# Kernel optimization log

Measured on AMD Instinct MI355X. Metric: run time of the kernel, lower is better.

The kernel has to match this reference:

```python
import jax, jax.numpy as jnp
import numpy as np

POOL = 7
IMG_DIM = 1024.0
NUM_CLASSES = 81
EPS = 1e-3


def crop_and_resize(fmap, boxes, P):
    """TF-style crop_and_resize with extrapolation_value=0.
    fmap: [C,H,W] (all box_indices are 0 in the original), boxes: [R,4] normalized (y1,x1,y2,x2).
    Returns [R,C,P,P]."""
    C, H, W = fmap.shape
    y1, x1, y2, x2 = boxes[:, 0], boxes[:, 1], boxes[:, 2], boxes[:, 3]
    g = jnp.arange(P, dtype=fmap.dtype) / (P - 1)  # [P]
    ys = y1[:, None] * (H - 1) + g[None, :] * ((y2 - y1) * (H - 1))[:, None]  # [R,P]
    xs = x1[:, None] * (W - 1) + g[None, :] * ((x2 - x1) * (W - 1))[:, None]  # [R,P]

    def axis(coords, size):
        valid = (coords >= 0) & (coords <= size - 1)
        c = jnp.clip(coords, 0, size - 1)
        lo = jnp.floor(c)
        hi = jnp.minimum(lo + 1, size - 1)
        return lo.astype(jnp.int32), hi.astype(jnp.int32), c - lo, valid

    y_lo, y_hi, wy, vy = axis(ys, H)
    x_lo, x_hi, wx, vx = axis(xs, W)

    def gather(yi, xi):  # -> [C,R,P,P]
        return fmap[:, yi[:, :, None], xi[:, None, :]]

    wxe = wx[None, :, None, :]
    top = gather(y_lo, x_lo) * (1 - wxe) + gather(y_lo, x_hi) * wxe
    bot = gather(y_hi, x_lo) * (1 - wxe) + gather(y_hi, x_hi) * wxe
    wye = wy[None, :, :, None]
    out = top * (1 - wye) + bot * wye
    mask = (vy[:, :, None] & vx[:, None, :])[None]  # [1,R,P,P]
    out = jnp.where(mask, out, jnp.zeros((), fmap.dtype))
    return jnp.transpose(out, (1, 0, 2, 3))  # [R,C,P,P]


def roi_align(fmaps, rois_flat):
    """rois_flat: [R,4] pixel coords (x1,y1,x2,y2). fmaps: list of 4 [C,H,W] (levels 2..5)."""
    x1, y1, x2, y2 = rois_flat[:, 0], rois_flat[:, 1], rois_flat[:, 2], rois_flat[:, 3]
    s = jnp.sqrt(jnp.maximum((y2 - y1) * (x2 - x1), 0.0))
    roi_level = jnp.log(s / 224.0) / np.log(2.0)
    roi_level = jnp.clip(jnp.round(roi_level) + 4, 2, 5)  # [R]
    boxes_norm = (rois_flat / IMG_DIM)[:, [1, 0, 3, 2]]  # (y1,x1,y2,x2)
    pooled = jnp.zeros((rois_flat.shape[0], fmaps[0].shape[0], POOL, POOL), rois_flat.dtype)
    for i, level in enumerate(range(2, 6)):
        crops = crop_and_resize(fmaps[i], boxes_norm, POOL)  # [R,C,P,P]
        sel = (roi_level == level)[:, None, None, None]
        pooled = jnp.where(sel, crops, pooled)
    return pooled  # [R,C,P,P]


def bn(x, g, b, m, v):  # inference batchnorm over channel axis (last)
    return (x - m) * (g / jnp.sqrt(v + EPS)) + b


def head(pooled, conv1_w, conv1_b, bn1_g, bn1_b, bn1_m, bn1_v,
         conv2_w, conv2_b, bn2_g, bn2_b, bn2_m, bn2_v,
         logits_w, logits_b, bbox_w, bbox_b):
    # conv1: 7x7 'valid' conv collapsing spatial dims -> dense [R,1024]
    x = jnp.einsum('rchw,kchw->rk', pooled, conv1_w) + conv1_b
    x = jax.nn.relu(bn(x, bn1_g, bn1_b, bn1_m, bn1_v))
    x = x @ conv2_w.T + conv2_b  # 1x1 conv == matmul
    shared = jax.nn.relu(bn(x, bn2_g, bn2_b, bn2_m, bn2_v))
    logits = shared @ logits_w.T + logits_b          # [R,NC]
    probs = jax.nn.softmax(logits, axis=-1)
    bbox = (shared @ bbox_w.T + bbox_b).reshape(-1, NUM_CLASSES, 4)
    return logits, probs, bbox


def setup_inputs() -> dict:
    key = jax.random.key(0)
    ks = jax.random.split(key, 24)
    B, N, C = 1, 1000, 256
    d = {}
    sizes = [256, 128, 64, 32]
    for i, s in enumerate(sizes):
        d[f'p{i+2}'] = jax.random.normal(ks[i], (B, C, s, s), jnp.float32)
    # valid boxes in pixel coords (x1,y1,x2,y2) spanning all pyramid levels
    cx = jax.random.uniform(ks[4], (B, N), minval=100.0, maxval=924.0)
    cy = jax.random.uniform(ks[5], (B, N), minval=100.0, maxval=924.0)
    hw = jax.random.uniform(ks[6], (B, N), minval=8.0, maxval=400.0)
    hh = jax.random.uniform(ks[7], (B, N), minval=8.0, maxval=400.0)
    rois = jnp.stack([jnp.clip(cx - hw, 0, 1024), jnp.clip(cy - hh, 0, 1024),
                      jnp.clip(cx + hw, 0, 1024), jnp.clip(cy + hh, 0, 1024)], axis=-1)
    d['rois'] = rois.astype(jnp.float32)
    sc = 0.02
    d['conv1_w'] = jax.random.normal(ks[8], (1024, 256, POOL, POOL)) * sc
    d['conv1_b'] = jnp.zeros((1024,), jnp.float32)
    d['bn1_g'] = jnp.ones((1024,), jnp.float32)
    d['bn1_b'] = jnp.zeros((1024,), jnp.float32)
    d['bn1_m'] = jnp.zeros((1024,), jnp.float32)
    d['bn1_v'] = jnp.ones((1024,), jnp.float32)
    d['conv2_w'] = jax.random.normal(ks[9], (1024, 1024)) * sc
    d['conv2_b'] = jnp.zeros((1024,), jnp.float32)
    d['bn2_g'] = jnp.ones((1024,), jnp.float32)
    d['bn2_b'] = jnp.zeros((1024,), jnp.float32)
    d['bn2_m'] = jnp.zeros((1024,), jnp.float32)
    d['bn2_v'] = jnp.ones((1024,), jnp.float32)
    d['logits_w'] = jax.random.normal(ks[10], (NUM_CLASSES, 1024)) * sc
    d['logits_b'] = jnp.zeros((NUM_CLASSES,), jnp.float32)
    d['bbox_w'] = jax.random.normal(ks[11], (NUM_CLASSES * 4, 1024)) * sc
    d['bbox_b'] = jnp.zeros((NUM_CLASSES * 4,), jnp.float32)
    return d


def reference(p2, p3, p4, p5, rois,
              conv1_w, conv1_b, bn1_g, bn1_b, bn1_m, bn1_v,
              conv2_w, conv2_b, bn2_g, bn2_b, bn2_m, bn2_v,
              logits_w, logits_b, bbox_w, bbox_b):
    B, N = rois.shape[0], rois.shape[1]
    fmaps = [p2[0], p3[0], p4[0], p5[0]]  # box_indices are all 0 in the original
    rois_flat = rois.reshape(B * N, 4)
    pooled = roi_align(fmaps, rois_flat)  # [B*N,256,7,7]
    logits, probs, bbox = head(pooled, conv1_w, conv1_b, bn1_g, bn1_b, bn1_m, bn1_v,
                               conv2_w, conv2_b, bn2_g, bn2_b, bn2_m, bn2_v,
                               logits_w, logits_b, bbox_w, bbox_b)
    return (logits.reshape(B, N, NUM_CLASSES),
            probs.reshape(B, N, NUM_CLASSES),
            bbox.reshape(B, N, NUM_CLASSES, 4))
```

## Files before the change

kernel.cpp:

```cpp
#include <hip/hip_runtime.h>
#include <hip/hip_fp16.h>
#include <math.h>

typedef _Float16 f16;
typedef _Float16 half8 __attribute__((ext_vector_type(8)));
typedef _Float16 half4v __attribute__((ext_vector_type(4)));
typedef _Float16 half2v __attribute__((ext_vector_type(2)));
typedef float f32x4 __attribute__((ext_vector_type(4)));


__device__ __forceinline__ void gload16(const f16* g, f16* lds) {
  __builtin_amdgcn_global_load_lds(
      (const __attribute__((address_space(1))) unsigned int*)g,
      (__attribute__((address_space(3))) unsigned int*)lds, 16, 0, 0);
}

__device__ __forceinline__ void fmap_body(int b, f16* tile,
                                          const float* __restrict__ p3,
                                          const float* __restrict__ p4,
                                          const float* __restrict__ p5,
                                          f16* __restrict__ dst0) {
  const float* src;
  int Ppix, p0;
  size_t dstoff;
  if (b < 128)      { src = p3; Ppix = 16384; dstoff = 0;     p0 = b * 128; }
  else if (b < 160) { src = p4; Ppix = 4096;  dstoff = 16384; p0 = (b - 128) * 128; }
  else              { src = p5; Ppix = 1024;  dstoff = 20480; p0 = (b - 160) * 128; }
  const int t = threadIdx.x;
  const int px4 = (t & 31) * 4;
  const int cp = (t >> 5) * 2;
#pragma unroll 4
  for (int i = 0; i < 16; i++) {
    const int c = i * 16 + cp;
    const float4 va = *(const float4*)&src[(size_t)c * Ppix + p0 + px4];
    const float4 vb = *(const float4*)&src[(size_t)(c + 1) * Ppix + p0 + px4];
    const float a_[4] = {va.x, va.y, va.z, va.w};
    const float b_[4] = {vb.x, vb.y, vb.z, vb.w};
#pragma unroll
    for (int j = 0; j < 4; j++) {
      const int px = px4 + j;
      const int cs = c ^ (((px >> 2) & 31) << 3);
      half2v h = {(f16)a_[j], (f16)b_[j]};
      *(half2v*)&tile[px * 256 + cs] = h;
    }
  }
  __syncthreads();
  f16* d = dst0 + (dstoff + (size_t)p0) * 256;
  const int c8 = (t & 31) * 8;
#pragma unroll 4
  for (int i = 0; i < 16; i++) {
    const int px = (t >> 5) * 16 + i;
    const int c8s = c8 ^ (((px >> 2) & 31) << 3);
    const half8 o = *(const half8*)&tile[px * 256 + c8s];
    *(half8*)&d[px * 256 + c8] = o;
  }
}

__device__ __forceinline__ void w1t_body(int k, f16* tile,
                                         const float* __restrict__ w1,
                                         f16* __restrict__ w1t) {
  const int t = threadIdx.x;
  const float* src = w1 + (size_t)k * 12544;
  f16* dst = w1t + (size_t)k * 12544;
#pragma unroll 7
  for (int i = 0; i < 49; i++) {
    const int idx = i * 256 + t;
    const int c = idx / 49, pq = idx % 49;
    tile[pq * 260 + c] = (f16)src[idx];
  }
  __syncthreads();
#pragma unroll
  for (int i = 0; i < 7; i++) {
    const int h8 = i * 256 + t;
    if (h8 < 1568) {
      const int pq = h8 >> 5, c8 = (h8 & 31) * 8;
      const half4v lo = *(const half4v*)&tile[pq * 260 + c8];
      const half4v hi = *(const half4v*)&tile[pq * 260 + c8 + 4];
      half8 o;
      o[0] = lo[0]; o[1] = lo[1]; o[2] = lo[2]; o[3] = lo[3];
      o[4] = hi[0]; o[5] = hi[1]; o[6] = hi[2]; o[7] = hi[3];
      *(half8*)&dst[pq * 256 + c8] = o;
    }
  }
}

__global__ __launch_bounds__(256) void prep_big_k(const float* __restrict__ p3,
                                                  const float* __restrict__ p4,
                                                  const float* __restrict__ p5,
                                                  const float* __restrict__ conv1_w,
                                                  f16* __restrict__ fmapT,
                                                  f16* __restrict__ w1t) {
  __shared__ __align__(16) f16 buf[32768];
  const int bid = blockIdx.x;
  const int g = bid / 7, r = bid % 7;
  if (r == 0) {
    if (g < 168) fmap_body(g, buf, p3, p4, p5, fmapT);
  } else {
    const int wb = g * 6 + (r - 1);
    if (wb < 1024) w1t_body(wb, buf, conv1_w, w1t);
  }
}

__global__ void prep_small_k(const float* __restrict__ conv2_w,
                             const float* __restrict__ lw, const float* __restrict__ lb,
                             const float* __restrict__ bw, const float* __restrict__ bb,
                             f16* __restrict__ w2t, f16* __restrict__ wcat,
                             float* __restrict__ bcat) {
  const int i = blockIdx.x * 256 + threadIdx.x;
  if (i < 262144) {
    const float4 v = ((const float4*)conv2_w)[i];
    half4v o = {(f16)v.x, (f16)v.y, (f16)v.z, (f16)v.w};
    ((half4v*)w2t)[i] = o;
  } else if (i < 262144 + 131072) {
    const int idx4 = i - 262144;
    const int elem = idx4 * 4;
    const int row = elem >> 10, col = elem & 1023;
    half4v o;
#pragma unroll
    for (int j = 0; j < 4; j++) {
      float v = 0.f;
      if (row < 81) v = lw[row * 1024 + col + j];
      else if (row < 405) v = bw[(row - 81) * 1024 + col + j];
      o[j] = (f16)v;
    }
    ((half4v*)wcat)[idx4] = o;
  } else if (i < 262144 + 131072 + 128) {
    const int j = (i - 393216) * 4;
    float r[4];
#pragma unroll
    for (int q = 0; q < 4; q++) {
      const int c = j + q;
      float bv = 0.f;
      if (c < 81) bv = lb[c];
      else if (c < 405) bv = bb[c - 81];
      r[q] = bv;
    }
    float4 o;
    o.x = r[0]; o.y = r[1]; o.z = r[2]; o.w = r[3];
    *(float4*)&bcat[j] = o;
  }
}

__global__ __launch_bounds__(256) void roi_align_k(const float* __restrict__ rois,
                                                   const float* __restrict__ p2,
                                                   const f16* __restrict__ fmapT,
                                                   f16* __restrict__ pooled) {
  const int t = threadIdx.x;
  __shared__ f16 ot[49 * 257];
  if (blockIdx.x >= 1024) {
    const int r = blockIdx.x - 1024;
    if (r >= 1000) return;
    const float x1 = rois[r * 4 + 0], y1 = rois[r * 4 + 1];
    const float x2 = rois[r * 4 + 2], y2 = rois[r * 4 + 3];
    const float s = sqrtf(fmaxf((y2 - y1) * (x2 - x1), 0.f));
    const float lf = logf(s / 224.0f) / 0.69314718055994531f;
    int lv = (int)rintf(lf) + 4;
    lv = lv < 2 ? 2 : (lv > 5 ? 5 : lv);
    if (lv != 2) return;
    const int wid = t >> 6, lane = t & 63;
    const float Hm1 = 255.f;
    int o00 = 0, o01 = 0, o10 = 0, o11 = 0;
    float wxl = 0.f, wyl = 0.f;
    bool vv = false;
    if (lane < 49) {
      const int py = lane / 7, px = lane % 7;
      const float y1n = y1 * (1.0f / 1024.0f), y2n = y2 * (1.0f / 1024.0f);
      const float x1n = x1 * (1.0f / 1024.0f), x2n = x2 * (1.0f / 1024.0f);
      const float cyc = y1n * Hm1 + ((float)py / 6.0f) * ((y2n - y1n) * Hm1);
      const float cxc = x1n * Hm1 + ((float)px / 6.0f) * ((x2n - x1n) * Hm1);
      const bool vy = (cyc >= 0.f) && (cyc <= Hm1);
      const bool vx = (cxc >= 0.f) && (cxc <= Hm1);
      float cy = fminf(fmaxf(cyc, 0.f), Hm1);
      float cx = fminf(fmaxf(cxc, 0.f), Hm1);
      const float fy = floorf(cy), fx = floorf(cx);
      const int ylo = (int)fy, xlo = (int)fx;
      const int yhi = (int)fminf(fy + 1.f, Hm1);
      const int xhi = (int)fminf(fx + 1.f, Hm1);
      wyl = cy - fy;
      wxl = cx - fx;
      vv = vy && vx;
      o00 = ylo * 256 + xlo;
      o01 = ylo * 256 + xhi;
      o10 = yhi * 256 + xlo;
      o11 = yhi * 256 + xhi;
    }
#pragma unroll 4
    for (int ci = 0; ci < 64; ci++) {
      const int ch = ci * 4 + wid;
      const float* pc = p2 + (size_t)ch * 65536;
      if (lane < 49) {
        const float v00 = pc[o00], v01 = pc[o01];
        const float v10 = pc[o10], v11 = pc[o11];
        const float top = v00 * (1.f - wxl) + v01 * wxl;
        const float bot = v10 * (1.f - wxl) + v11 * wxl;
        float val = top * (1.f - wyl) + bot * wyl;
        if (!vv) val = 0.f;
        ot[lane * 257 + ch] = (f16)val;
      }
    }
    __syncthreads();
    f16* outp = pooled + (size_t)r * 12544;
#pragma unroll 7
    for (int pos = 0; pos < 49; pos++) outp[pos * 256 + t] = ot[pos * 257 + t];
    return;
  }
  const int r = blockIdx.x;
  if (r >= 1000) {
    f16* outp = pooled + (size_t)r * 12544;
#pragma unroll 7
    for (int i = 0; i < 49; i++) outp[i * 256 + t] = (f16)0.f;
    return;
  }
  __shared__ int s_lo[14], s_hi[14], s_val[14];
  __shared__ float s_w[14];
  __shared__ int q00[49], q01[49], q10[49], q11[49], qv[49];
  __shared__ float qwx[49], qwy[49];
  const float x1 = rois[r * 4 + 0], y1 = rois[r * 4 + 1];
  const float x2 = rois[r * 4 + 2], y2 = rois[r * 4 + 3];
  const float s = sqrtf(fmaxf((y2 - y1) * (x2 - x1), 0.f));
  const float lf = logf(s / 224.0f) / 0.69314718055994531f;
  int lv = (int)rintf(lf) + 4;
  lv = lv < 2 ? 2 : (lv > 5 ? 5 : lv);
  const int li = lv - 2;
  if (li == 0) return;
  const int H = 256 >> li;
  const int off = (li == 1) ? 0 : (li == 2) ? 16384 : 20480;
  const float Hm1 = (float)(H - 1);
  if (t < 14) {
    const bool isx = t >= 7;
    const int i = isx ? t - 7 : t;
    const float b1 = (isx ? x1 : y1) * (1.0f / 1024.0f);
    const float b2 = (isx ? x2 : y2) * (1.0f / 1024.0f);
    const float g = (float)i / 6.0f;
    const float coord = b1 * Hm1 + g * ((b2 - b1) * Hm1);
    const int valid = (coord >= 0.f) && (coord <= Hm1);
    float c = fminf(fmaxf(coord, 0.f), Hm1);
    float lo = floorf(c);
    s_lo[t] = (int)lo;
    s_hi[t] = (int)fminf(lo + 1.f, Hm1);
    s_w[t] = c - lo;
    s_val[t] = valid;
  }
  __syncthreads();
  if (t < 49) {
    const int py = t / 7, px = t - py * 7;
    const int ylo = s_lo[py], yhi = s_hi[py];
    const int xlo = s_lo[7 + px], xhi = s_hi[7 + px];
    q00[t] = (ylo * H + xlo) * 256;
    q01[t] = (ylo * H + xhi) * 256;
    q10[t] = (yhi * H + xlo) * 256;
    q11[t] = (yhi * H + xhi) * 256;
    qwx[t] = s_w[7 + px];
    qwy[t] = s_w[py];
    qv[t] = s_val[py] && s_val[7 + px];
  }
  __syncthreads();
  const int c8 = (t & 31) * 8;
  const int g = t >> 5;
  const f16* base = fmapT + (size_t)off * 256 + c8;
  f16* outp = pooled + (size_t)r * 12544 + c8;
#pragma unroll
  for (int i = 0; i < 7; i++) {
    const int pos = g + i * 8;
    if (pos < 49) {
      const half8 v00 = *(const half8*)&base[q00[pos]];
      const half8 v01 = *(const half8*)&base[q01[pos]];
      const half8 v10 = *(const half8*)&base[q10[pos]];
      const half8 v11 = *(const half8*)&base[q11[pos]];
      const float wx = qwx[pos], wy = qwy[pos];
      const bool ok = qv[pos];
      half8 o;
#pragma unroll
      for (int q = 0; q < 8; q++) {
        const float top = (float)v00[q] * (1.f - wx) + (float)v01[q] * wx;
        const float bot = (float)v10[q] * (1.f - wx) + (float)v11[q] * wx;
        float vv = top * (1.f - wy) + bot * wy;
        if (!ok) vv = 0.f;
        o[q] = (f16)vv;
      }
      *(half8*)&outp[pos * 256] = o;
    }
  }
}

__global__ __launch_bounds__(512) void gemm1_d2(
    const f16* __restrict__ A, const f16* __restrict__ B, float* __restrict__ part,
    int K, int kPerSplit) {
  __shared__ __align__(16) f16 As[4][256 * 32];
  __shared__ __align__(16) f16 Bs[4][128 * 32];
  const int t = threadIdx.x;

  int lid = blockIdx.x + 8 * (blockIdx.y + 4 * blockIdx.z);
  const int chunk = (8 * 4 * (int)gridDim.z) >> 3;
  lid = (lid & 7) * chunk + (lid >> 3);
  const int bx = lid & 7;
  const int by = (lid >> 3) & 3;
  const int bz = lid >> 5;

  const int m0 = by * 256, n0 = bx * 128;
  const int wid = t >> 6, lane = t & 63;
  const int wr = (wid & 3) * 64;
  const int wc = (wid >> 2) * 64;
  const int lrow = lane & 15;
  const int lsl = lane >> 4;
  const int srow = t >> 2;
  const int scol = (((t & 3) ^ ((t >> 3) & 3)) << 3);
  const int kz0 = bz * kPerSplit;
  const int nIter = kPerSplit >> 5;

  f32x4 acc[4][4] = {};
  const f16* Ab = A + (size_t)(m0 + srow) * K + kz0 + scol;
  const f16* Bb = B + (size_t)(n0 + srow) * K + kz0 + scol;
  f16* asb = &As[0][0] + wid * 512;
  f16* bsb = &Bs[0][0] + wid * 512;

#define STG(kt) do {                                                           \
    const int sl_ = (kt) & 3; const size_t ko_ = (size_t)(kt) * 32;            \
    gload16(Ab + ko_, asb + sl_ * 8192);                                       \
    gload16(Ab + (size_t)128 * K + ko_, asb + sl_ * 8192 + 4096);              \
    gload16(Bb + ko_, bsb + sl_ * 4096);                                       \
    __builtin_amdgcn_sched_barrier(0);                                         \
  } while (0)

  STG(0);
  STG(1);
  asm volatile("s_waitcnt vmcnt(3)" ::: "memory");
  __builtin_amdgcn_sched_barrier(0);
  __builtin_amdgcn_s_barrier();

  for (int kt = 0; kt < nIter; ++kt) {
    const int sl = kt & 3;
    const f16* as = &As[sl][0];
    const f16* bs = &Bs[sl][0];
    half8 aF[4], bF[4];
#pragma unroll
    for (int m = 0; m < 4; m++) {
      const int r_ = wr + m * 16 + lrow;
      aF[m] = *(const half8*)&as[r_ * 32 + ((lsl ^ ((r_ >> 1) & 3)) << 3)];
    }
#pragma unroll
    for (int n = 0; n < 4; n++) {
      const int r_ = wc + n * 16 + lrow;
      bF[n] = *(const half8*)&bs[r_ * 32 + ((lsl ^ ((r_ >> 1) & 3)) << 3)];
    }
    if (kt + 2 < nIter) STG(kt + 2);
    __builtin_amdgcn_s_setprio(1);
#pragma unroll
    for (int m = 0; m < 4; m++)
#pragma unroll
      for (int n = 0; n < 4; n++)
        acc[m][n] = __builtin_amdgcn_mfma_f32_16x16x32_f16(aF[m], bF[n], acc[m][n], 0, 0, 0);
    __builtin_amdgcn_s_setprio(0);
    if (kt + 2 < nIter) { asm volatile("s_waitcnt vmcnt(3)" ::: "memory"); }
    else                { asm volatile("s_waitcnt vmcnt(0)" ::: "memory"); }
    __builtin_amdgcn_sched_barrier(0);
    __builtin_amdgcn_s_barrier();
  }
#undef STG

  float* outp = part + (size_t)bz * (1024 * 1024);
#pragma unroll
  for (int m = 0; m < 4; m++) {
    const int rr = m0 + wr + m * 16 + lsl * 4;
#pragma unroll
    for (int n = 0; n < 4; n++) {
      const int cc = n0 + wc + n * 16 + lrow;
#pragma unroll
      for (int j = 0; j < 4; j++)
        outp[(size_t)(rr + j) * 1024 + cc] = acc[m][n][j];
    }
  }
}

__global__ __launch_bounds__(256) void gemm_nt_p3(
    const f16* __restrict__ A, const f16* __restrict__ B, float* __restrict__ part,
    int K, int kPerSplit, int ldc) {
  __shared__ __align__(16) f16 As[3][128 * 32];
  __shared__ __align__(16) f16 Bs[3][128 * 32];
  const int t = threadIdx.x;

  const int gx = gridDim.x, gy = gridDim.y;
  int lid = blockIdx.x + gx * (blockIdx.y + gy * blockIdx.z);
  const int chunk = (gx * gy * (int)gridDim.z) >> 3;
  lid = (lid & 7) * chunk + (lid >> 3);
  const int bx = lid % gx;
  const int tmp = lid / gx;
  const int by = tmp % gy;
  const int bz = tmp / gy;

  const int m0 = by * 128;
  const int n0 = bx * 128;
  const int wid = t >> 6;
  const int lane = t & 63;
  const int wr = (wid >> 1) * 64;
  const int wc = (wid & 1) * 64;
  const int lrow = lane & 15;
  const int lsl = lane >> 4;
  const int rowA = t >> 2;
  const int c8 = (((t & 3) ^ ((rowA >> 1) & 3)) << 3);
  const int kz0 = bz * kPerSplit;
  const int nIter = kPerSplit >> 5;

  f32x4 acc[4][4] = {};
  const f16* Ab = A + (size_t)m0 * K + kz0 + c8;
  const f16* Bb = B + (size_t)n0 * K + kz0 + c8;

#define STAGE(buf, it)                                                        \
  do {                                                                        \
    const int ko = (it) * 32;                                                 \
    gload16(Ab + (size_t)rowA * K + ko, &As[buf][wid * 512]);                 \
    gload16(Ab + (size_t)(rowA + 64) * K + ko, &As[buf][2048 + wid * 512]);   \
    gload16(Bb + (size_t)rowA * K + ko, &Bs[buf][wid * 512]);                 \
    gload16(Bb + (size_t)(rowA + 64) * K + ko, &Bs[buf][2048 + wid * 512]);   \
  } while (0)

#define COMPUTE(buf)                                                          \
  do {                                                                        \
    half8 aF[4], bF[4];                                                       \
    _Pragma("unroll") for (int m = 0; m < 4; m++) {                           \
      const int rr_ = wr + m * 16 + lrow;                                     \
      aF[m] = *(const half8*)&As[buf][rr_ * 32 + ((lsl ^ ((rr_ >> 1) & 3)) << 3)]; \
    }                                                                         \
    _Pragma("unroll") for (int n = 0; n < 4; n++) {                           \
      const int rr_ = wc + n * 16 + lrow;                                     \
      bF[n] = *(const half8*)&Bs[buf][rr_ * 32 + ((lsl ^ ((rr_ >> 1) & 3)) << 3)]; \
    }                                                                         \
    __builtin_amdgcn_s_setprio(1);                                            \
    _Pragma("unroll") for (int m = 0; m < 4; m++)                             \
      _Pragma("unroll") for (int n = 0; n < 4; n++)                           \
        acc[m][n] = __builtin_amdgcn_mfma_f32_16x16x32_f16(aF[m], bF[n], acc[m][n], 0, 0, 0); \
    __builtin_amdgcn_s_setprio(0);                                            \
  } while (0)

  STAGE(0, 0);
  STAGE(1, 1);
  int bc = 0;
  for (int it = 0; it < nIter - 2; ++it) {
    const int bs_ = (bc == 0) ? 2 : bc - 1;
    STAGE(bs_, it + 2);
    asm volatile("s_waitcnt vmcnt(8)" ::: "memory");
    __builtin_amdgcn_sched_barrier(0);
    __builtin_amdgcn_s_barrier();
    COMPUTE(bc);
    __builtin_amdgcn_s_barrier();
    bc = (bc == 2) ? 0 : bc + 1;
  }
  asm volatile("s_waitcnt vmcnt(4)" ::: "memory");
  __builtin_amdgcn_sched_barrier(0);
  __builtin_amdgcn_s_barrier();
  COMPUTE(bc);
  __builtin_amdgcn_s_barrier();
  bc = (bc == 2) ? 0 : bc + 1;
  asm volatile("s_waitcnt vmcnt(0)" ::: "memory");
  __builtin_amdgcn_sched_barrier(0);
  __builtin_amdgcn_s_barrier();
  COMPUTE(bc);
#undef STAGE
#undef COMPUTE

  const size_t slice = (size_t)gy * 128 * ldc;
#pragma unroll
  for (int m = 0; m < 4; m++) {
#pragma unroll
    for (int n = 0; n < 4; n++) {
#pragma unroll
      for (int j = 0; j < 4; j++) {
        const int rr = m0 + wr + m * 16 + ((lane >> 4) << 2) + j;
        const int cc = n0 + wc + n * 16 + (lane & 15);
        part[(size_t)bz * slice + (size_t)rr * ldc + cc] = acc[m][n][j];
      }
    }
  }
}

template <int Z>
__global__ void reduce_ep_k(const float* __restrict__ part, int sliceE, int ldc,
                            const float* __restrict__ bias, const float* __restrict__ g,
                            const float* __restrict__ b, const float* __restrict__ m,
                            const float* __restrict__ v, f16* __restrict__ out) {
  const int i4 = (blockIdx.x * 256 + threadIdx.x) * 4;
  float4 s = *(const float4*)(part + i4);
#pragma unroll
  for (int z = 1; z < Z; z++) {
    const float4 p = *(const float4*)(part + (size_t)z * sliceE + i4);
    s.x += p.x; s.y += p.y; s.z += p.z; s.w += p.w;
  }
  const int c0 = i4 % ldc;
  float r[4] = {s.x, s.y, s.z, s.w};
  half4v o;
#pragma unroll
  for (int j = 0; j < 4; j++) {
    const int c = c0 + j;
    const float x = r[j] + bias[c];
    const float sc = g[c] / sqrtf(v[c] + 1e-3f);
    o[j] = (f16)fmaxf((x - m[c]) * sc + b[c], 0.f);
  }
  *(half4v*)(out + i4) = o;
}

__global__ __launch_bounds__(256) void reduce3_out_k(const float* __restrict__ part,
                                                     const float* __restrict__ bcat,
                                                     float* __restrict__ out) {
  const int r = blockIdx.x, t = threadIdx.x;
  __shared__ float red[256];
  const float* base = part + (size_t)r * 512;
  float v0 = 0.f, v1 = 0.f;
  {
    float s = bcat[t];
#pragma unroll
    for (int z = 0; z < 8; z++) s += base[(size_t)z * 524288 + t];
    v0 = s;
  }
  if (t < 149) {
    float s = bcat[256 + t];
#pragma unroll
    for (int z = 0; z < 8; z++) s += base[(size_t)z * 524288 + 256 + t];
    v1 = s;
  }
  red[t] = (t < 81) ? v0 : -INFINITY;
  __syncthreads();
  for (int s_ = 128; s_ > 0; s_ >>= 1) {
    if (t < s_) red[t] = fmaxf(red[t], red[t + s_]);
    __syncthreads();
  }
  const float mx = red[0];
  __syncthreads();
  const float e = (t < 81) ? expf(v0 - mx) : 0.f;
  red[t] = e;
  __syncthreads();
  for (int s_ = 128; s_ > 0; s_ >>= 1) {
    if (t < s_) red[t] += red[t + s_];
    __syncthreads();
  }
  const float inv = 1.f / red[0];
  if (t < 81) {
    out[(size_t)r * 81 + t] = v0;
    out[81000 + (size_t)r * 81 + t] = e * inv;
  }
  if (t >= 81) out[162000 + (size_t)r * 324 + (t - 81)] = v0;
  if (t < 149) out[162000 + (size_t)r * 324 + 175 + t] = v1;
}

extern "C" void kernel_launch(void* const* d_in, const int* in_sizes, int n_in,
                              void* d_out, int out_size, void* d_ws, size_t ws_size,
                              hipStream_t stream) {
  const float* p2 = (const float*)d_in[0];
  const float* p3 = (const float*)d_in[1];
  const float* p4 = (const float*)d_in[2];
  const float* p5 = (const float*)d_in[3];
  const float* rois = (const float*)d_in[4];
  const float* conv1_w = (const float*)d_in[5];
  const float* conv1_b = (const float*)d_in[6];
  const float* bn1_g = (const float*)d_in[7];
  const float* bn1_b = (const float*)d_in[8];
  const float* bn1_m = (const float*)d_in[9];
  const float* bn1_v = (const float*)d_in[10];
  const float* conv2_w = (const float*)d_in[11];
  const float* conv2_b = (const float*)d_in[12];
  const float* bn2_g = (const float*)d_in[13];
  const float* bn2_b = (const float*)d_in[14];
  const float* bn2_m = (const float*)d_in[15];
  const float* bn2_v = (const float*)d_in[16];
  const float* logits_w = (const float*)d_in[17];
  const float* logits_b = (const float*)d_in[18];
  const float* bbox_w = (const float*)d_in[19];
  const float* bbox_b = (const float*)d_in[20];

  char* ws = (char*)d_ws;
  f16* sh1 = (f16*)(ws + (size_t)0);
  f16* sh2 = (f16*)(ws + ((size_t)2 << 20));
  f16* w2t = (f16*)(ws + ((size_t)6 << 20));
  f16* wcat = (f16*)(ws + ((size_t)8 << 20));
  float* bcat = (float*)(ws + ((size_t)9 << 20));
  f16* fmapT = (f16*)(ws + (size_t)9961472);
  float* part = (float*)(ws + ((size_t)10 << 20));
  f16* pooled = (f16*)(ws + (size_t)44564480);
  f16* w1t = (f16*)(ws + (size_t)70254592);

  prep_small_k<<<1537, 256, 0, stream>>>(conv2_w, logits_w, logits_b, bbox_w, bbox_b,
                                         w2t, wcat, bcat);
  prep_big_k<<<1197, 256, 0, stream>>>(p3, p4, p5, conv1_w, fmapT, w1t);
  roi_align_k<<<2024, 256, 0, stream>>>(rois, p2, fmapT, pooled);
  gemm1_d2<<<dim3(8, 4, 8), 512, 0, stream>>>(pooled, w1t, part, 12544, 1568);
  reduce_ep_k<8><<<1024, 256, 0, stream>>>(part, 1048576, 1024, conv1_b, bn1_g,
                                           bn1_b, bn1_m, bn1_v, sh1);
  gemm_nt_p3<<<dim3(8, 8, 4), 256, 0, stream>>>(sh1, w2t, part, 1024, 256, 1024);
  reduce_ep_k<4><<<1024, 256, 0, stream>>>(part, 1048576, 1024, conv2_b, bn2_g,
                                           bn2_b, bn2_m, bn2_v, sh2);
  gemm_nt_p3<<<dim3(4, 8, 8), 256, 0, stream>>>(sh2, wcat, part, 1024, 128, 512);
  reduce3_out_k<<<1000, 256, 0, stream>>>(part, bcat, (float*)d_out);
}
```

Measured before the change: 124.2 us.

## Move level-2 ROI align into prep kernel and split remaining ROI blocks

Level-2 ROI align, which reads p2 directly, now runs inside the prep_big_k launch alongside the fmap transpose and w1 conversion blocks, so it overlaps with that work instead of waiting for it. The remaining levels (3-5) get their own kernel that splits each ROI across two blocks covering 25 and 24 positions. That kernel also hoists all four sets of gather loads ahead of the compute, behind a sched_barrier, to increase memory-level parallelism. The combined prep kernel uses more shared memory per block and has uneven per-block work, which could hurt scheduling.

```diff
diff --git a/kernel.cpp b/kernel.cpp
--- a/kernel.cpp
+++ b/kernel.cpp
@@ -84,72 +84,20 @@
   }
 }
 
-__global__ __launch_bounds__(256) void prep_big_k(const float* __restrict__ p3,
+__global__ __launch_bounds__(256) void prep_big_k(const float* __restrict__ p2,
+                                                  const float* __restrict__ p3,
                                                   const float* __restrict__ p4,
                                                   const float* __restrict__ p5,
                                                   const float* __restrict__ conv1_w,
+                                                  const float* __restrict__ rois,
                                                   f16* __restrict__ fmapT,
-                                                  f16* __restrict__ w1t) {
+                                                  f16* __restrict__ w1t,
+                                                  f16* __restrict__ pooled) {
   __shared__ __align__(16) f16 buf[32768];
   const int bid = blockIdx.x;
-  const int g = bid / 7, r = bid % 7;
-  if (r == 0) {
-    if (g < 168) fmap_body(g, buf, p3, p4, p5, fmapT);
-  } else {
-    const int wb = g * 6 + (r - 1);
-    if (wb < 1024) w1t_body(wb, buf, conv1_w, w1t);
-  }
-}
-
-__global__ void prep_small_k(const float* __restrict__ conv2_w,
-                             const float* __restrict__ lw, const float* __restrict__ lb,
-                             const float* __restrict__ bw, const float* __restrict__ bb,
-                             f16* __restrict__ w2t, f16* __restrict__ wcat,
-                             float* __restrict__ bcat) {
-  const int i = blockIdx.x * 256 + threadIdx.x;
-  if (i < 262144) {
-    const float4 v = ((const float4*)conv2_w)[i];
-    half4v o = {(f16)v.x, (f16)v.y, (f16)v.z, (f16)v.w};
-    ((half4v*)w2t)[i] = o;
-  } else if (i < 262144 + 131072) {
-    const int idx4 = i - 262144;
-    const int elem = idx4 * 4;
-    const int row = elem >> 10, col = elem & 1023;
-    half4v o;
-#pragma unroll
-    for (int j = 0; j < 4; j++) {
-      float v = 0.f;
-      if (row < 81) v = lw[row * 1024 + col + j];
-      else if (row < 405) v = bw[(row - 81) * 1024 + col + j];
-      o[j] = (f16)v;
-    }
-    ((half4v*)wcat)[idx4] = o;
-  } else if (i < 262144 + 131072 + 128) {
-    const int j = (i - 393216) * 4;
-    float r[4];
-#pragma unroll
-    for (int q = 0; q < 4; q++) {
-      const int c = j + q;
-      float bv = 0.f;
-      if (c < 81) bv = lb[c];
-      else if (c < 405) bv = bb[c - 81];
-      r[q] = bv;
-    }
-    float4 o;
-    o.x = r[0]; o.y = r[1]; o.z = r[2]; o.w = r[3];
-    *(float4*)&bcat[j] = o;
-  }
-}
-
-__global__ __launch_bounds__(256) void roi_align_k(const float* __restrict__ rois,
-                                                   const float* __restrict__ p2,
-                                                   const f16* __restrict__ fmapT,
-                                                   f16* __restrict__ pooled) {
   const int t = threadIdx.x;
-  __shared__ f16 ot[49 * 257];
-  if (blockIdx.x >= 1024) {
-    const int r = blockIdx.x - 1024;
-    if (r >= 1000) return;
+  if (bid < 1000) {
+    const int r = bid;
     const float x1 = rois[r * 4 + 0], y1 = rois[r * 4 + 1];
     const float x2 = rois[r * 4 + 2], y2 = rois[r * 4 + 3];
     const float s = sqrtf(fmaxf((y2 - y1) * (x2 - x1), 0.f));
@@ -195,26 +143,82 @@
         const float bot = v10 * (1.f - wxl) + v11 * wxl;
         float val = top * (1.f - wyl) + bot * wyl;
         if (!vv) val = 0.f;
-        ot[lane * 257 + ch] = (f16)val;
+        buf[lane * 257 + ch] = (f16)val;
       }
     }
     __syncthreads();
     f16* outp = pooled + (size_t)r * 12544;
 #pragma unroll 7
-    for (int pos = 0; pos < 49; pos++) outp[pos * 256 + t] = ot[pos * 257 + t];
+    for (int pos = 0; pos < 49; pos++) outp[pos * 256 + t] = buf[pos * 257 + t];
     return;
   }
-  const int r = blockIdx.x;
+  const int b2 = bid - 1000;
+  const int g = b2 / 7, rr = b2 % 7;
+  if (rr == 0) {
+    if (g < 168) fmap_body(g, buf, p3, p4, p5, fmapT);
+  } else {
+    const int wb = g * 6 + (rr - 1);
+    if (wb < 1024) w1t_body(wb, buf, conv1_w, w1t);
+  }
+}
+
+__global__ void prep_small_k(const float* __restrict__ conv2_w,
+                             const float* __restrict__ lw, const float* __restrict__ lb,
+                             const float* __restrict__ bw, const float* __restrict__ bb,
+                             f16* __restrict__ w2t, f16* __restrict__ wcat,
+                             float* __restrict__ bcat) {
+  const int i = blockIdx.x * 256 + threadIdx.x;
+  if (i < 262144) {
+    const float4 v = ((const float4*)conv2_w)[i];
+    half4v o = {(f16)v.x, (f16)v.y, (f16)v.z, (f16)v.w};
+    ((half4v*)w2t)[i] = o;
+  } else if (i < 262144 + 131072) {
+    const int idx4 = i - 262144;
+    const int elem = idx4 * 4;
+    const int row = elem >> 10, col = elem & 1023;
+    half4v o;
+#pragma unroll
+    for (int j = 0; j < 4; j++) {
+      float v = 0.f;
+      if (row < 81) v = lw[row * 1024 + col + j];
+      else if (row < 405) v = bw[(row - 81) * 1024 + col + j];
+      o[j] = (f16)v;
+    }
+    ((half4v*)wcat)[idx4] = o;
+  } else if (i < 262144 + 131072 + 128) {
+    const int j = (i - 393216) * 4;
+    float r[4];
+#pragma unroll
+    for (int q = 0; q < 4; q++) {
+      const int c = j + q;
+      float bv = 0.f;
+      if (c < 81) bv = lb[c];
+      else if (c < 405) bv = bb[c - 81];
+      r[q] = bv;
+    }
+    float4 o;
+    o.x = r[0]; o.y = r[1]; o.z = r[2]; o.w = r[3];
+    *(float4*)&bcat[j] = o;
+  }
+}
+
+__global__ __launch_bounds__(256) void roi_norm_k(const float* __restrict__ rois,
+                                                  const f16* __restrict__ fmapT,
+                                                  f16* __restrict__ pooled) {
+  const int bid = blockIdx.x;
+  const int r = bid >> 1, h = bid & 1;
+  const int t = threadIdx.x;
+  const int npos = h ? 24 : 25;
+  const int pbase = h ? 25 : 0;
   if (r >= 1000) {
-    f16* outp = pooled + (size_t)r * 12544;
-#pragma unroll 7
-    for (int i = 0; i < 49; i++) outp[i * 256 + t] = (f16)0.f;
+    f16* outp = pooled + (size_t)r * 12544 + t;
+    for (int i = 0; i < npos; i++) outp[(pbase + i) * 256] = (f16)0.f;
     return;
   }
   __shared__ int s_lo[14], s_hi[14], s_val[14];
   __shared__ float s_w[14];
-  __shared__ int q00[49], q01[49], q10[49], q11[49], qv[49];
-  __shared__ float qwx[49], qwy[49];
+  __shared__ int q00[25], q01[25], q10[25], q11[25], qv[25];
+  __shared__ float qwx[25], qwy[25];
   const float x1 = rois[r * 4 + 0], y1 = rois[r * 4 + 1];
   const float x2 = rois[r * 4 + 2], y2 = rois[r * 4 + 3];
   const float s = sqrtf(fmaxf((y2 - y1) * (x2 - x1), 0.f));
@@ -242,14 +246,13 @@
     s_val[t] = valid;
   }
   __syncthreads();
-  if (t < 49) {
-    const int py = t / 7, px = t - py * 7;
-    const int ylo = s_lo[py], yhi = s_hi[py];
-    const int xlo = s_lo[7 + px], xhi = s_hi[7 + px];
-    q00[t] = (ylo * H + xlo) * 256;
-    q01[t] = (ylo * H + xhi) * 256;
-    q10[t] = (yhi * H + xlo) * 256;
-    q11[t] = (yhi * H + xhi) * 256;
+  if (t < npos) {
+    const int pos = pbase + t;
+    const int py = pos / 7, px = pos - py * 7;
+    q00[t] = (s_lo[py] * H + s_lo[7 + px]) * 256;
+    q01[t] = (s_lo[py] * H + s_hi[7 + px]) * 256;
+    q10[t] = (s_hi[py] * H + s_lo[7 + px]) * 256;
+    q11[t] = (s_hi[py] * H + s_hi[7 + px]) * 256;
     qwx[t] = s_w[7 + px];
     qwy[t] = s_w[py];
     qv[t] = s_val[py] && s_val[7 + px];
@@ -259,26 +262,39 @@
   const int g = t >> 5;
   const f16* base = fmapT + (size_t)off * 256 + c8;
   f16* outp = pooled + (size_t)r * 12544 + c8;
-#pragma unroll
-  for (int i = 0; i < 7; i++) {
-    const int pos = g + i * 8;
-    if (pos < 49) {
-      const half8 v00 = *(const half8*)&base[q00[pos]];
-      const half8 v01 = *(const half8*)&base[q01[pos]];
-      const half8 v10 = *(const half8*)&base[q10[pos]];
-      const half8 v11 = *(const half8*)&base[q11[pos]];
-      const float wx = qwx[pos], wy = qwy[pos];
-      const bool ok = qv[pos];
+  int o00[4], o01[4], o10[4], o11[4], pw[4], ok[4], act[4];
+  float wx[4], wy[4];
+#pragma unroll
+  for (int i = 0; i < 4; i++) {
+    const int j = g + i * 8;
+    act[i] = (j < npos);
+    const int jj = act[i] ? j : 0;
+    o00[i] = q00[jj]; o01[i] = q01[jj]; o10[i] = q10[jj]; o11[i] = q11[jj];
+    wx[i] = qwx[jj]; wy[i] = qwy[jj]; ok[i] = qv[jj];
+    pw[i] = (pbase + jj) * 256;
+  }
+  half8 v00[4], v01[4], v10[4], v11[4];
+#pragma unroll
+  for (int i = 0; i < 4; i++) {
+    v00[i] = *(const half8*)&base[o00[i]];
+    v01[i] = *(const half8*)&base[o01[i]];
+    v10[i] = *(const half8*)&base[o10[i]];
+    v11[i] = *(const half8*)&base[o11[i]];
+  }
+  __builtin_amdgcn_sched_barrier(0);
+#pragma unroll
+  for (int i = 0; i < 4; i++) {
+    if (act[i]) {
       half8 o;
 #pragma unroll
       for (int q = 0; q < 8; q++) {
-        const float top = (float)v00[q] * (1.f - wx) + (float)v01[q] * wx;
-        const float bot = (float)v10[q] * (1.f - wx) + (float)v11[q] * wx;
-        float vv = top * (1.f - wy) + bot * wy;
-        if (!ok) vv = 0.f;
-        o[q] = (f16)vv;
+        const float top = (float)v00[i][q] * (1.f - wx[i]) + (float)v01[i][q] * wx[i];
+        const float bot = (float)v10[i][q] * (1.f - wx[i]) + (float)v11[i][q] * wx[i];
+        float vvq = top * (1.f - wy[i]) + bot * wy[i];
+        if (!ok[i]) vvq = 0.f;
+        o[q] = (f16)vvq;
       }
-      *(half8*)&outp[pos * 256] = o;
+      *(half8*)&outp[pw[i]] = o;
     }
   }
 }
@@ -579,8 +595,9 @@
 
   prep_small_k<<<1537, 256, 0, stream>>>(conv2_w, logits_w, logits_b, bbox_w, bbox_b,
                                          w2t, wcat, bcat);
-  prep_big_k<<<1197, 256, 0, stream>>>(p3, p4, p5, conv1_w, fmapT, w1t);
-  roi_align_k<<<2024, 256, 0, stream>>>(rois, p2, fmapT, pooled);
+  prep_big_k<<<2197, 256, 0, stream>>>(p2, p3, p4, p5, conv1_w, rois,
+                                       fmapT, w1t, pooled);
+  roi_norm_k<<<2048, 256, 0, stream>>>(rois, fmapT, pooled);
   gemm1_d2<<<dim3(8, 4, 8), 512, 0, stream>>>(pooled, w1t, part, 12544, 1568);
   reduce_ep_k<8><<<1024, 256, 0, stream>>>(part, 1048576, 1024, conv1_b, bn1_g,
                                            bn1_b, bn1_m, bn1_v, sh1);
```

Result: faster. 119.9 us (-3.5%).
